# Optimization experiments

Hardware: AMD Instinct MI355X
Metric: run time of the kernel (lower is better)

Reference implementation:

```python
import jax, jax.numpy as jnp
import numpy as np

B, S, D, H = 8, 1024, 1024, 16
HD = D // H
EPS = 1e-5

def layernorm(x, g, b):
    mu = jnp.mean(x, axis=-1, keepdims=True)
    var = jnp.mean(jnp.square(x - mu), axis=-1, keepdims=True)
    return (x - mu) * jax.lax.rsqrt(var + EPS) * g + b

def setup_inputs() -> dict:
    key = jax.random.key(0)
    ks = jax.random.split(key, 8)
    s = 0.02
    return {
        "x": jax.random.normal(ks[0], (B, S, D), jnp.float32),
        "mask": jnp.tril(jnp.ones((S, S), jnp.int32)),  # causal mask
        "ln1_g": jnp.ones((D,), jnp.float32),
        "ln1_b": jnp.zeros((D,), jnp.float32),
        "wqkv": jax.random.normal(ks[1], (D, 3 * D), jnp.float32) * s,
        "bqkv": jnp.zeros((3 * D,), jnp.float32),
        "wo": jax.random.normal(ks[2], (D, D), jnp.float32) * s,
        "bo": jnp.zeros((D,), jnp.float32),
        "ln2_g": jnp.ones((D,), jnp.float32),
        "ln2_b": jnp.zeros((D,), jnp.float32),
        "w1": jax.random.normal(ks[3], (D, 4 * D), jnp.float32) * s,
        "b1": jnp.zeros((4 * D,), jnp.float32),
        "w2": jax.random.normal(ks[4], (4 * D, D), jnp.float32) * s,
        "b2": jnp.zeros((D,), jnp.float32),
    }

def reference(x, mask, ln1_g, ln1_b, wqkv, bqkv, wo, bo, ln2_g, ln2_b, w1, b1, w2, b2):
    # --- pre-LN attention ---
    h = layernorm(x, ln1_g, ln1_b)
    qkv = h @ wqkv + bqkv                                  # [B,S,3D]
    qkv = qkv.reshape(B, S, 3, H, HD).transpose(2, 0, 3, 1, 4)
    q, k, v = qkv[0], qkv[1], qkv[2]                       # [B,H,S,HD]
    scores = jnp.einsum('bhqd,bhkd->bhqk', q, k) / jnp.sqrt(jnp.float32(HD))
    scores = jnp.where(mask == 0, -jnp.inf, scores)
    attn = jax.nn.softmax(scores, axis=-1)
    out = jnp.einsum('bhqk,bhkd->bhqd', attn, v)           # [B,H,S,HD]
    out = out.transpose(0, 2, 1, 3).reshape(B, S, D)
    x = x + (out @ wo + bo)
    # --- pre-LN MLP ---
    h = layernorm(x, ln2_g, ln2_b)
    h = jax.nn.gelu(h @ w1 + b1, approximate=False)
    x = x + (h @ w2 + b2)
    return x
```

## Files before the change

### kernel.cpp

```cpp
#include <hip/hip_runtime.h>


#define DEV static __device__ __forceinline__

typedef __attribute__((ext_vector_type(8))) __bf16 bf16x8;
typedef __attribute__((ext_vector_type(4))) float f32x4;

DEV ushort f2bf(float f) {
  union { float f; unsigned u; } c; c.f = f;
  unsigned r = (c.u + 0x7FFFu + ((c.u >> 16) & 1u)) >> 16;
  return (ushort)r;
}

DEV float geluf(float v) {
  return 0.5f * v * (1.0f + erff(v * 0.70710678118654752f));
}

__global__ __launch_bounds__(256)
void ln_bf16_kernel(const float* __restrict__ x, const float* __restrict__ g,
                    const float* __restrict__ bb, ushort* __restrict__ out)
{
  const int row = blockIdx.x, tid = threadIdx.x;
  const float4 v = ((const float4*)x)[row * 256 + tid];
  float s = v.x + v.y + v.z + v.w;
  float sq = v.x * v.x + v.y * v.y + v.z * v.z + v.w * v.w;
#pragma unroll
  for (int off = 32; off >= 1; off >>= 1) {
    s += __shfl_xor(s, off, 64);
    sq += __shfl_xor(sq, off, 64);
  }
  __shared__ float ps[4], pq[4];
  if ((tid & 63) == 0) { ps[tid >> 6] = s; pq[tid >> 6] = sq; }
  __syncthreads();
  s = ps[0] + ps[1] + ps[2] + ps[3];
  sq = pq[0] + pq[1] + pq[2] + pq[3];
  const float mu = s * (1.0f / 1024.0f);
  const float rstd = rsqrtf(sq * (1.0f / 1024.0f) - mu * mu + 1e-5f);
  const float4 gv = ((const float4*)g)[tid];
  const float4 bv = ((const float4*)bb)[tid];
  ushort4 o;
  o.x = f2bf((v.x - mu) * rstd * gv.x + bv.x);
  o.y = f2bf((v.y - mu) * rstd * gv.y + bv.y);
  o.z = f2bf((v.z - mu) * rstd * gv.z + bv.z);
  o.w = f2bf((v.w - mu) * rstd * gv.w + bv.w);
  ((ushort4*)out)[row * 256 + tid] = o;
}

__global__ __launch_bounds__(256)
void tcvt_kernel(const float* __restrict__ in, ushort* __restrict__ out, int K, int N)
{
  __shared__ float tile[32][33];
  const int tx = threadIdx.x & 31, ty = threadIdx.x >> 5;
  const int n0 = blockIdx.x * 32, k0 = blockIdx.y * 32;
#pragma unroll
  for (int j = 0; j < 4; ++j)
    tile[ty + j * 8][tx] = in[(size_t)(k0 + ty + j * 8) * N + n0 + tx];
  __syncthreads();
#pragma unroll
  for (int j = 0; j < 4; ++j)
    out[(size_t)(n0 + ty + j * 8) * K + k0 + tx] = f2bf(tile[tx][ty + j * 8]);
}

template<int EPI>
__global__ __launch_bounds__(256)
void gemm_bf16(const ushort* __restrict__ A, const ushort* __restrict__ Bt,
               const float* __restrict__ bias, const float* __restrict__ resid,
               void* __restrict__ outp, int M, int N, int K)
{
  __shared__ ushort As[128][40];
  __shared__ ushort Bs[128][40];
  const int tid = threadIdx.x;
  const int lane = tid & 63, wave = tid >> 6;
  const int wm = wave >> 1, wn = wave & 1;
  const int grp = lane >> 4, r16 = lane & 15;
  const int bm = blockIdx.y * 128, bn = blockIdx.x * 128;
  const int srow = tid >> 1, schk = (tid & 1) * 16;
  const ushort* pa = A + (size_t)(bm + srow) * K + schk;
  const ushort* pb = Bt + (size_t)(bn + srow) * K + schk;

  f32x4 acc[4][4] = {};

  for (int k0 = 0; k0 < K; k0 += 32) {
    const int4 av0 = *(const int4*)(pa + k0);
    const int4 av1 = *(const int4*)(pa + k0 + 8);
    const int4 bv0 = *(const int4*)(pb + k0);
    const int4 bv1 = *(const int4*)(pb + k0 + 8);
    __syncthreads();
    *(int4*)&As[srow][schk]     = av0;
    *(int4*)&As[srow][schk + 8] = av1;
    *(int4*)&Bs[srow][schk]     = bv0;
    *(int4*)&Bs[srow][schk + 8] = bv1;
    __syncthreads();
    bf16x8 af[4], bfr[4];
#pragma unroll
    for (int m = 0; m < 4; ++m)
      af[m] = *(const bf16x8*)&As[wm * 64 + m * 16 + r16][grp * 8];
#pragma unroll
    for (int n = 0; n < 4; ++n)
      bfr[n] = *(const bf16x8*)&Bs[wn * 64 + n * 16 + r16][grp * 8];
#pragma unroll
    for (int m = 0; m < 4; ++m)
#pragma unroll
      for (int n = 0; n < 4; ++n)
        acc[m][n] = __builtin_amdgcn_mfma_f32_16x16x32_bf16(af[m], bfr[n], acc[m][n], 0, 0, 0);
  }

#pragma unroll
  for (int n = 0; n < 4; ++n) {
    const int col = bn + wn * 64 + n * 16 + r16;
    const float bval = bias[col];
#pragma unroll
    for (int m = 0; m < 4; ++m) {
      const int row0 = bm + wm * 64 + m * 16 + grp * 4;
#pragma unroll
      for (int r = 0; r < 4; ++r) {
        const size_t idx = (size_t)(row0 + r) * N + col;
        float v = acc[m][n][r] + bval;
        if (EPI == 1) v = geluf(v);
        if (EPI == 2) ((float*)outp)[idx] = v + resid[idx];
        else          ((ushort*)outp)[idx] = f2bf(v);
      }
    }
  }
}

__global__ __launch_bounds__(256)
void attn_kernel(const ushort* __restrict__ qkv, ushort* __restrict__ out)
{
  __shared__ ushort Ks[64][72];
  __shared__ ushort Vt[64][72];
  __shared__ ushort Ps[4][16][72];
  const int tid = threadIdx.x, lane = tid & 63, w = tid >> 6;
  const int grp = lane >> 4, r16 = lane & 15;
  const int qb = blockIdx.x, bh = blockIdx.y;
  const int b = bh >> 4, h = bh & 15;
  const size_t rowbase = (size_t)b * 1024;
  const int q0 = qb * 64 + w * 16;

  bf16x8 qf[2];
  {
    const ushort* qp = qkv + (rowbase + q0 + r16) * 3072 + h * 64;
    qf[0] = *(const bf16x8*)(qp + grp * 8);
    qf[1] = *(const bf16x8*)(qp + 32 + grp * 8);
  }

  f32x4 o[4] = {};
  float mrow[4] = {-1e30f, -1e30f, -1e30f, -1e30f};
  float lsum[4] = {0.f, 0.f, 0.f, 0.f};

  for (int kb = 0; kb <= qb; ++kb) {
    __syncthreads();
#pragma unroll
    for (int p = 0; p < 2; ++p) {
      const int c = p * 256 + tid;
      const int kv = c >> 3, hc = (c & 7) * 8;
      const ushort* kp = qkv + (rowbase + kb * 64 + kv) * 3072 + 1024 + h * 64 + hc;
      *(int4*)&Ks[kv][hc] = *(const int4*)kp;
      union { int4 v; ushort u[8]; } vv;
      vv.v = *(const int4*)(kp + 1024);
#pragma unroll
      for (int j = 0; j < 8; ++j) Vt[hc + j][kv] = vv.u[j];
    }
    __syncthreads();

    f32x4 s[4] = {};
#pragma unroll
    for (int t = 0; t < 4; ++t) {
#pragma unroll
      for (int f = 0; f < 2; ++f) {
        const bf16x8 kf = *(const bf16x8*)&Ks[t * 16 + r16][f * 32 + grp * 8];
        s[t] = __builtin_amdgcn_mfma_f32_16x16x32_bf16(qf[f], kf, s[t], 0, 0, 0);
      }
    }
#pragma unroll
    for (int t = 0; t < 4; ++t)
#pragma unroll
      for (int r = 0; r < 4; ++r) {
        float v = s[t][r] * 0.125f;
        if (kb == qb && (t * 16 + r16) > (w * 16 + grp * 4 + r)) v = -1e30f;
        s[t][r] = v;
      }
    float fac[4];
#pragma unroll
    for (int r = 0; r < 4; ++r) {
      float mx = fmaxf(fmaxf(s[0][r], s[1][r]), fmaxf(s[2][r], s[3][r]));
#pragma unroll
      for (int msk = 1; msk < 16; msk <<= 1) mx = fmaxf(mx, __shfl_xor(mx, msk, 16));
      const float mn = fmaxf(mrow[r], mx);
      fac[r] = __expf(mrow[r] - mn);
      mrow[r] = mn;
      lsum[r] *= fac[r];
    }
#pragma unroll
    for (int t = 0; t < 4; ++t)
#pragma unroll
      for (int r = 0; r < 4; ++r) o[t][r] *= fac[r];
    float rsum[4] = {0.f, 0.f, 0.f, 0.f};
#pragma unroll
    for (int t = 0; t < 4; ++t)
#pragma unroll
      for (int r = 0; r < 4; ++r) {
        const float p = __expf(s[t][r] - mrow[r]);
        s[t][r] = p;
        rsum[r] += p;
      }
#pragma unroll
    for (int r = 0; r < 4; ++r) {
#pragma unroll
      for (int msk = 1; msk < 16; msk <<= 1) rsum[r] += __shfl_xor(rsum[r], msk, 16);
      lsum[r] += rsum[r];
    }
#pragma unroll
    for (int t = 0; t < 4; ++t)
#pragma unroll
      for (int r = 0; r < 4; ++r)
        Ps[w][grp * 4 + r][t * 16 + r16] = f2bf(s[t][r]);
    __syncthreads();
    bf16x8 pf[2];
    pf[0] = *(const bf16x8*)&Ps[w][r16][grp * 8];
    pf[1] = *(const bf16x8*)&Ps[w][r16][32 + grp * 8];
#pragma unroll
    for (int t = 0; t < 4; ++t) {
#pragma unroll
      for (int f = 0; f < 2; ++f) {
        const bf16x8 vf = *(const bf16x8*)&Vt[t * 16 + r16][f * 32 + grp * 8];
        o[t] = __builtin_amdgcn_mfma_f32_16x16x32_bf16(pf[f], vf, o[t], 0, 0, 0);
      }
    }
  }

  float inv[4];
#pragma unroll
  for (int r = 0; r < 4; ++r) inv[r] = 1.0f / lsum[r];
#pragma unroll
  for (int t = 0; t < 4; ++t)
#pragma unroll
    for (int r = 0; r < 4; ++r) {
      const int qrow = qb * 64 + w * 16 + grp * 4 + r;
      out[(rowbase + qrow) * 1024 + h * 64 + t * 16 + r16] = f2bf(o[t][r] * inv[r]);
    }
}

extern "C" void kernel_launch(void* const* d_in, const int* in_sizes, int n_in,
                              void* d_out, int out_size, void* d_ws, size_t ws_size,
                              hipStream_t stream) {
  (void)in_sizes; (void)n_in; (void)out_size; (void)ws_size;
  const float* x     = (const float*)d_in[0];
  const float* ln1_g = (const float*)d_in[2];
  const float* ln1_b = (const float*)d_in[3];
  const float* wqkv  = (const float*)d_in[4];
  const float* bqkv  = (const float*)d_in[5];
  const float* wo    = (const float*)d_in[6];
  const float* bo    = (const float*)d_in[7];
  const float* ln2_g = (const float*)d_in[8];
  const float* ln2_b = (const float*)d_in[9];
  const float* w1    = (const float*)d_in[10];
  const float* b1    = (const float*)d_in[11];
  const float* w2    = (const float*)d_in[12];
  const float* b2    = (const float*)d_in[13];
  float* out = (float*)d_out;
  char* ws = (char*)d_ws;

  ushort* wqkvT = (ushort*)(ws + 0);
  ushort* woT   = (ushort*)(ws + 6291456);
  ushort* w1T   = (ushort*)(ws + 8388608);
  ushort* w2T   = (ushort*)(ws + 16777216);
  ushort* R1    = (ushort*)(ws + 25165824);
  ushort* R2    = (ushort*)(ws + 41943040);

  const dim3 blk(256);
  tcvt_kernel<<<dim3(3072 / 32, 1024 / 32), blk, 0, stream>>>(wqkv, wqkvT, 1024, 3072);
  tcvt_kernel<<<dim3(1024 / 32, 1024 / 32), blk, 0, stream>>>(wo, woT, 1024, 1024);
  tcvt_kernel<<<dim3(4096 / 32, 1024 / 32), blk, 0, stream>>>(w1, w1T, 1024, 4096);
  tcvt_kernel<<<dim3(1024 / 32, 4096 / 32), blk, 0, stream>>>(w2, w2T, 4096, 1024);

  ln_bf16_kernel<<<8192, blk, 0, stream>>>(x, ln1_g, ln1_b, R1);
  gemm_bf16<0><<<dim3(3072 / 128, 8192 / 128), blk, 0, stream>>>(R1, wqkvT, bqkv, nullptr, R2, 8192, 3072, 1024);
  attn_kernel<<<dim3(16, 128), blk, 0, stream>>>(R2, R1);
  gemm_bf16<2><<<dim3(1024 / 128, 8192 / 128), blk, 0, stream>>>(R1, woT, bo, x, out, 8192, 1024, 1024);
  ln_bf16_kernel<<<8192, blk, 0, stream>>>(out, ln2_g, ln2_b, R1);
  gemm_bf16<1><<<dim3(4096 / 128, 8192 / 128), blk, 0, stream>>>(R1, w1T, b1, nullptr, R2, 8192, 4096, 1024);
  gemm_bf16<2><<<dim3(1024 / 128, 8192 / 128), blk, 0, stream>>>(R2, w2T, b2, out, out, 8192, 1024, 4096);
}
```

Before: 678.0 us.

## Use direct global-to-LDS loads with swizzle in GEMM and pre-transpose V for attention

The GEMM now stages A/B tiles with global_load_lds straight into an XOR-swizzled LDS layout, with a K-step of 64 instead of 32. The aim is fewer register round trips, half as many barriers and fewer bank conflicts. A separate kernel pre-transposes V into a [bh][hd][s] buffer. The attention kernel then reads K and V^T fragments directly from global memory, dropping the LDS staging and the block-wide syncs. This trades shared-memory reuse across the four waves for uncoalesced global fragment loads, adds an extra launch, and removes a sync around the per-wave P buffer.

```diff
diff --git a/kernel.cpp b/kernel.cpp
--- a/kernel.cpp
+++ b/kernel.cpp
@@ -14,6 +14,12 @@
 
 DEV float geluf(float v) {
   return 0.5f * v * (1.0f + erff(v * 0.70710678118654752f));
+}
+
+DEV void gload16(const ushort* g, ushort* l) {
+  __builtin_amdgcn_global_load_lds(
+      (const __attribute__((address_space(1))) void*)g,
+      (__attribute__((address_space(3))) void*)l, 16, 0, 0);
 }
 
 __global__ __launch_bounds__(256)
@@ -61,48 +67,81 @@
     out[(size_t)(n0 + ty + j * 8) * K + k0 + tx] = f2bf(tile[tx][ty + j * 8]);
 }
 
+__global__ __launch_bounds__(256)
+void vtr_kernel(const ushort* __restrict__ qkv, ushort* __restrict__ VT)
+{
+  __shared__ ushort tile[64][72];
+  const int tid = threadIdx.x;
+  const int bh = blockIdx.x, sb = blockIdx.y;
+  const int b = bh >> 4, h = bh & 15;
+  const int s0 = sb * 64;
+#pragma unroll
+  for (int it = 0; it < 2; ++it) {
+    const int idx = it * 256 + tid;
+    const int r = idx >> 3, hc = (idx & 7) * 8;
+    *(int4*)&tile[r][hc] =
+        *(const int4*)(qkv + ((size_t)b * 1024 + s0 + r) * 3072 + 2048 + h * 64 + hc);
+  }
+  __syncthreads();
+#pragma unroll
+  for (int it = 0; it < 2; ++it) {
+    const int idx = it * 256 + tid;
+    const int hd = idx >> 3, sc = (idx & 7) * 8;
+    union { int4 v; ushort u[8]; } o;
+#pragma unroll
+    for (int j = 0; j < 8; ++j) o.u[j] = tile[sc + j][hd];
+    *(int4*)(VT + ((size_t)bh * 64 + hd) * 1024 + s0 + sc) = o.v;
+  }
+}
+
 template<int EPI>
 __global__ __launch_bounds__(256)
 void gemm_bf16(const ushort* __restrict__ A, const ushort* __restrict__ Bt,
                const float* __restrict__ bias, const float* __restrict__ resid,
                void* __restrict__ outp, int M, int N, int K)
 {
-  __shared__ ushort As[128][40];
-  __shared__ ushort Bs[128][40];
+  __shared__ ushort Asl[128 * 64];
+  __shared__ ushort Bsl[128 * 64];
   const int tid = threadIdx.x;
-  const int lane = tid & 63, wave = tid >> 6;
-  const int wm = wave >> 1, wn = wave & 1;
+  const int lane = tid & 63, w = tid >> 6;
+  const int wm = w >> 1, wn = w & 1;
   const int grp = lane >> 4, r16 = lane & 15;
   const int bm = blockIdx.y * 128, bn = blockIdx.x * 128;
-  const int srow = tid >> 1, schk = (tid & 1) * 16;
-  const ushort* pa = A + (size_t)(bm + srow) * K + schk;
-  const ushort* pb = Bt + (size_t)(bn + srow) * K + schk;
+
+  const int lrow = lane >> 3;
+  const int uswz = ((lane & 7) ^ lrow) * 8;
+  const ushort* pa = A  + (size_t)(bm + w * 32 + lrow) * K + uswz;
+  const ushort* pb = Bt + (size_t)(bn + w * 32 + lrow) * K + uswz;
 
   f32x4 acc[4][4] = {};
 
-  for (int k0 = 0; k0 < K; k0 += 32) {
-    const int4 av0 = *(const int4*)(pa + k0);
-    const int4 av1 = *(const int4*)(pa + k0 + 8);
-    const int4 bv0 = *(const int4*)(pb + k0);
-    const int4 bv1 = *(const int4*)(pb + k0 + 8);
+  for (int k0 = 0; k0 < K; k0 += 64) {
     __syncthreads();
-    *(int4*)&As[srow][schk]     = av0;
-    *(int4*)&As[srow][schk + 8] = av1;
-    *(int4*)&Bs[srow][schk]     = bv0;
-    *(int4*)&Bs[srow][schk + 8] = bv1;
+#pragma unroll
+    for (int i = 0; i < 4; ++i) {
+      gload16(pa + (size_t)(i * 8) * K + k0, &Asl[(w * 32 + i * 8) * 64]);
+      gload16(pb + (size_t)(i * 8) * K + k0, &Bsl[(w * 32 + i * 8) * 64]);
+    }
     __syncthreads();
-    bf16x8 af[4], bfr[4];
-#pragma unroll
-    for (int m = 0; m < 4; ++m)
-      af[m] = *(const bf16x8*)&As[wm * 64 + m * 16 + r16][grp * 8];
-#pragma unroll
-    for (int n = 0; n < 4; ++n)
-      bfr[n] = *(const bf16x8*)&Bs[wn * 64 + n * 16 + r16][grp * 8];
-#pragma unroll
-    for (int m = 0; m < 4; ++m)
-#pragma unroll
-      for (int n = 0; n < 4; ++n)
-        acc[m][n] = __builtin_amdgcn_mfma_f32_16x16x32_bf16(af[m], bfr[n], acc[m][n], 0, 0, 0);
+#pragma unroll
+    for (int ks = 0; ks < 2; ++ks) {
+      bf16x8 af[4], bfr[4];
+#pragma unroll
+      for (int m = 0; m < 4; ++m) {
+        const int r = wm * 64 + m * 16 + r16;
+        af[m] = *(const bf16x8*)&Asl[r * 64 + ((ks * 4 + grp) ^ (r16 & 7)) * 8];
+      }
+#pragma unroll
+      for (int n = 0; n < 4; ++n) {
+        const int r = wn * 64 + n * 16 + r16;
+        bfr[n] = *(const bf16x8*)&Bsl[r * 64 + ((ks * 4 + grp) ^ (r16 & 7)) * 8];
+      }
+#pragma unroll
+      for (int m = 0; m < 4; ++m)
+#pragma unroll
+        for (int n = 0; n < 4; ++n)
+          acc[m][n] = __builtin_amdgcn_mfma_f32_16x16x32_bf16(af[m], bfr[n], acc[m][n], 0, 0, 0);
+    }
   }
 
 #pragma unroll
@@ -125,10 +164,9 @@
 }
 
 __global__ __launch_bounds__(256)
-void attn_kernel(const ushort* __restrict__ qkv, ushort* __restrict__ out)
-{
-  __shared__ ushort Ks[64][72];
-  __shared__ ushort Vt[64][72];
+void attn_kernel(const ushort* __restrict__ qkv, const ushort* __restrict__ VT,
+                 ushort* __restrict__ out)
+{
   __shared__ ushort Ps[4][16][72];
   const int tid = threadIdx.x, lane = tid & 63, w = tid >> 6;
   const int grp = lane >> 4, r16 = lane & 15;
@@ -143,32 +181,21 @@
     qf[0] = *(const bf16x8*)(qp + grp * 8);
     qf[1] = *(const bf16x8*)(qp + 32 + grp * 8);
   }
+  const ushort* kbase = qkv + rowbase * 3072 + 1024 + h * 64;
+  const ushort* vbase = VT + (size_t)bh * 64 * 1024;
 
   f32x4 o[4] = {};
   float mrow[4] = {-1e30f, -1e30f, -1e30f, -1e30f};
   float lsum[4] = {0.f, 0.f, 0.f, 0.f};
 
   for (int kb = 0; kb <= qb; ++kb) {
-    __syncthreads();
-#pragma unroll
-    for (int p = 0; p < 2; ++p) {
-      const int c = p * 256 + tid;
-      const int kv = c >> 3, hc = (c & 7) * 8;
-      const ushort* kp = qkv + (rowbase + kb * 64 + kv) * 3072 + 1024 + h * 64 + hc;
-      *(int4*)&Ks[kv][hc] = *(const int4*)kp;
-      union { int4 v; ushort u[8]; } vv;
-      vv.v = *(const int4*)(kp + 1024);
-#pragma unroll
-      for (int j = 0; j < 8; ++j) Vt[hc + j][kv] = vv.u[j];
-    }
-    __syncthreads();
-
     f32x4 s[4] = {};
 #pragma unroll
     for (int t = 0; t < 4; ++t) {
 #pragma unroll
       for (int f = 0; f < 2; ++f) {
-        const bf16x8 kf = *(const bf16x8*)&Ks[t * 16 + r16][f * 32 + grp * 8];
+        const bf16x8 kf = *(const bf16x8*)(kbase +
+            (size_t)(kb * 64 + t * 16 + r16) * 3072 + f * 32 + grp * 8);
         s[t] = __builtin_amdgcn_mfma_f32_16x16x32_bf16(qf[f], kf, s[t], 0, 0, 0);
       }
     }
@@ -215,7 +242,6 @@
 #pragma unroll
       for (int r = 0; r < 4; ++r)
         Ps[w][grp * 4 + r][t * 16 + r16] = f2bf(s[t][r]);
-    __syncthreads();
     bf16x8 pf[2];
     pf[0] = *(const bf16x8*)&Ps[w][r16][grp * 8];
     pf[1] = *(const bf16x8*)&Ps[w][r16][32 + grp * 8];
@@ -223,7 +249,8 @@
     for (int t = 0; t < 4; ++t) {
 #pragma unroll
       for (int f = 0; f < 2; ++f) {
-        const bf16x8 vf = *(const bf16x8*)&Vt[t * 16 + r16][f * 32 + grp * 8];
+        const bf16x8 vf = *(const bf16x8*)(vbase +
+            (size_t)(t * 16 + r16) * 1024 + kb * 64 + f * 32 + grp * 8);
         o[t] = __builtin_amdgcn_mfma_f32_16x16x32_bf16(pf[f], vf, o[t], 0, 0, 0);
       }
     }
@@ -267,6 +294,7 @@
   ushort* w2T   = (ushort*)(ws + 16777216);
   ushort* R1    = (ushort*)(ws + 25165824);
   ushort* R2    = (ushort*)(ws + 41943040);
+  ushort* VT    = (ushort*)(ws + 41943040 + 50331648);
 
   const dim3 blk(256);
   tcvt_kernel<<<dim3(3072 / 32, 1024 / 32), blk, 0, stream>>>(wqkv, wqkvT, 1024, 3072);
@@ -276,7 +304,8 @@
 
   ln_bf16_kernel<<<8192, blk, 0, stream>>>(x, ln1_g, ln1_b, R1);
   gemm_bf16<0><<<dim3(3072 / 128, 8192 / 128), blk, 0, stream>>>(R1, wqkvT, bqkv, nullptr, R2, 8192, 3072, 1024);
-  attn_kernel<<<dim3(16, 128), blk, 0, stream>>>(R2, R1);
+  vtr_kernel<<<dim3(128, 16), blk, 0, stream>>>(R2, VT);
+  attn_kernel<<<dim3(16, 128), blk, 0, stream>>>(R2, VT, R1);
   gemm_bf16<2><<<dim3(1024 / 128, 8192 / 128), blk, 0, stream>>>(R1, woT, bo, x, out, 8192, 1024, 1024);
   ln_bf16_kernel<<<8192, blk, 0, stream>>>(out, ln2_g, ln2_b, R1);
   gemm_bf16<1><<<dim3(4096 / 128, 8192 / 128), blk, 0, stream>>>(R1, w1T, b1, nullptr, R2, 8192, 4096, 1024);
```

Result: no change. 668.0 us (-1.5%).
